# Kernel tuning notes

Measured on AMD Instinct MI355X. Metric: run time of the kernel, lower is better.

## Reference

```python
import jax, jax.numpy as jnp
import numpy as np

ALPHA = 1.5
DIM = -1
N_ITER = 50


def setup_inputs() -> dict:
    key = jax.random.key(0)
    X = jax.random.normal(key, (4096, 32000), dtype=jnp.float32)
    return {"X": X}


def reference(X):
    alpha = ALPHA
    d = X.shape[DIM]
    inv = 1.0 / (alpha - 1.0)  # exponent 1/(alpha-1)

    max_val = jnp.max(X, axis=DIM, keepdims=True)
    Xs = X * (alpha - 1.0)
    max_val = max_val * (alpha - 1.0)

    tau_lo = max_val - 1.0
    tau_hi = max_val - (1.0 / d) ** (alpha - 1.0)
    dm = tau_hi - tau_lo

    def body(i, carry):
        tau_lo, dm, _ = carry
        dm = dm * 0.5
        tau_m = tau_lo + dm
        p_m = jnp.clip(Xs - tau_m, 0.0) ** inv
        f_m = jnp.sum(p_m, axis=DIM, keepdims=True) - 1.0
        tau_lo = jnp.where(f_m >= 0.0, tau_m, tau_lo)
        return (tau_lo, dm, tau_m)

    tau_lo, dm, tau_m = jax.lax.fori_loop(0, N_ITER, body, (tau_lo, dm, tau_lo))
    # p_m from the last iteration's tau_m (matches torch loop semantics)
    p_m = jnp.clip(Xs - tau_m, 0.0) ** inv
    # ensure_sum_one=True
    p_m = p_m / jnp.sum(p_m, axis=DIM, keepdims=True)
    return p_m
```

## Files before the change

### kernel.cpp

```cpp
#include <hip/hip_runtime.h>
#include <cstdint>
#include <cstddef>


#define DLEN    32000
#define NCHUNK  8000
#define BLOCK   1024
#define PER_T   8
#define RPB     16
#define GRID_B  256
#define CAP     2048

__device__ __forceinline__ void async_copy16(void* lds_dst, const void* gsrc) {
  __builtin_amdgcn_global_load_lds(
      (const __attribute__((address_space(1))) void*)gsrc,
      (__attribute__((address_space(3))) void*)lds_dst,
      16, 0, 0);
}

__global__ __launch_bounds__(BLOCK) void entmax_bisect_kernel(
    const float* __restrict__ X, float* __restrict__ out) {
  __shared__ alignas(16) float rowbuf[DLEN];
  __shared__ float cand[CAP];
  __shared__ float wmax[BLOCK / 64];
  __shared__ int   cnt;

  const int t    = threadIdx.x;
  const int lane = t & 63;
  const int blk  = blockIdx.x;

  {
    const float* src = X + (size_t)blk * DLEN;
#pragma unroll
    for (int j = 0; j < PER_T; ++j) {
      const int c = t + j * BLOCK;
      if (c < NCHUNK) async_copy16(&rowbuf[c * 4], src + (size_t)c * 4);
    }
  }

  for (int r = 0; r < RPB; ++r) {
    const size_t row = (size_t)blk + (size_t)r * GRID_B;

    asm volatile("s_waitcnt vmcnt(0)" ::: "memory");
    __syncthreads();

    float4 v[PER_T];
#pragma unroll
    for (int j = 0; j < PER_T; ++j) {
      const int c = t + j * BLOCK;
      if (c < NCHUNK) {
        float4 q = *reinterpret_cast<const float4*>(&rowbuf[c * 4]);
        q.x *= 0.5f; q.y *= 0.5f; q.z *= 0.5f; q.w *= 0.5f;
        v[j] = q;
      } else {
        v[j] = make_float4(-3.4e38f, -3.4e38f, -3.4e38f, -3.4e38f);
      }
    }
    __syncthreads();

    if (t == 0) cnt = 0;

    if (r + 1 < RPB) {
      const float* src = X + ((size_t)blk + (size_t)(r + 1) * GRID_B) * DLEN;
#pragma unroll
      for (int j = 0; j < PER_T; ++j) {
        const int c = t + j * BLOCK;
        if (c < NCHUNK) async_copy16(&rowbuf[c * 4], src + (size_t)c * 4);
      }
    }

    float m = -3.4e38f;
#pragma unroll
    for (int j = 0; j < PER_T; ++j)
      m = fmaxf(m, fmaxf(fmaxf(v[j].x, v[j].y), fmaxf(v[j].z, v[j].w)));
#pragma unroll
    for (int off = 32; off > 0; off >>= 1) m = fmaxf(m, __shfl_xor(m, off));
    if (lane == 0) wmax[t >> 6] = m;
    __syncthreads();

    float ms = wmax[0];
#pragma unroll
    for (int w = 1; w < BLOCK / 64; ++w) ms = fmaxf(ms, wmax[w]);

    const float tlo0 = ms - 1.0f;

#pragma unroll
    for (int j = 0; j < PER_T; ++j) {
      if (v[j].x > tlo0) { int i = atomicAdd(&cnt, 1); if (i < CAP) cand[i] = v[j].x; }
      if (v[j].y > tlo0) { int i = atomicAdd(&cnt, 1); if (i < CAP) cand[i] = v[j].y; }
      if (v[j].z > tlo0) { int i = atomicAdd(&cnt, 1); if (i < CAP) cand[i] = v[j].z; }
      if (v[j].w > tlo0) { int i = atomicAdd(&cnt, 1); if (i < CAP) cand[i] = v[j].w; }
    }
    __syncthreads();

    int nc = cnt;
    if (nc > CAP) nc = CAP;

    float tau_lo = tlo0;
    float dm     = (ms - 0.0055901699437494745f) - tau_lo;
    float tau_m  = tau_lo;

#pragma unroll 1
    for (int it = 0; it < 50; ++it) {
      dm *= 0.5f;
      tau_m = tau_lo + dm;
      float s = 0.0f;
      for (int k = lane; k < nc; k += 64) {
        float d0 = fmaxf(cand[k] - tau_m, 0.0f);
        s += d0 * d0;
      }
#pragma unroll
      for (int off = 32; off > 0; off >>= 1) s += __shfl_xor(s, off);
      if (s - 1.0f >= 0.0f) tau_lo = tau_m;
      if (it < 49 && (tau_lo + dm * 0.5f == tau_lo)) { tau_m = tau_lo; break; }
    }

    float s = 0.0f;
    for (int k = lane; k < nc; k += 64) {
      float d0 = fmaxf(cand[k] - tau_m, 0.0f);
      s += d0 * d0;
    }
#pragma unroll
    for (int off = 32; off > 0; off >>= 1) s += __shfl_xor(s, off);
    const float inv_sum = 1.0f / s;

    float* dst = out + row * DLEN;
#pragma unroll
    for (int j = 0; j < PER_T; ++j) {
      const int c = t + j * BLOCK;
      if (c < NCHUNK) {
        const float4 q = v[j];
        float4 o;
        float d0;
        d0 = q.x - tau_m; o.x = (d0 > 0.0f) ? d0 * d0 * inv_sum : 0.0f;
        d0 = q.y - tau_m; o.y = (d0 > 0.0f) ? d0 * d0 * inv_sum : 0.0f;
        d0 = q.z - tau_m; o.z = (d0 > 0.0f) ? d0 * d0 * inv_sum : 0.0f;
        d0 = q.w - tau_m; o.w = (d0 > 0.0f) ? d0 * d0 * inv_sum : 0.0f;
        *reinterpret_cast<float4*>(dst + (size_t)c * 4) = o;
      }
    }
  }
}

extern "C" void kernel_launch(void* const* d_in, const int* in_sizes, int n_in,
                              void* d_out, int out_size, void* d_ws, size_t ws_size,
                              hipStream_t stream) {
  (void)in_sizes; (void)n_in; (void)d_ws; (void)ws_size; (void)out_size;
  const float* X = (const float*)d_in[0];
  float* out = (float*)d_out;
  entmax_bisect_kernel<<<dim3(GRID_B), dim3(BLOCK), 0, stream>>>(X, out);
}
```

Measured before the change: 1.080 ms.

## Replace LDS row prefetch with direct loads, doubled grid, and wave-scan candidate compaction

Drops the async global-to-LDS row prefetch and loads each row straight into registers. The grid doubles to 512 blocks with 8 rows each, and the 125KB row buffer is gone, so LDS use per block shrinks and more blocks can be resident. Candidate compaction now counts per thread, runs a wave prefix scan and issues one LDS atomic per wave, replacing one atomic per element. The change gives up explicit prefetch overlap and relies on occupancy to hide load latency. It also raises the candidate cap.

```diff
diff --git a/kernel.cpp b/kernel.cpp
--- a/kernel.cpp
+++ b/kernel.cpp
@@ -3,93 +3,79 @@
 #include <cstddef>
 
 
-#define DLEN    32000
-#define NCHUNK  8000
-#define BLOCK   1024
-#define PER_T   8
-#define RPB     16
-#define GRID_B  256
-#define CAP     2048
+#define DLEN   32000
+#define NCH    8000
+#define BLOCK  1024
+#define PER_T  8
+#define GRID_B 512
+#define RPB    8
+#define CAP    6144
 
-__device__ __forceinline__ void async_copy16(void* lds_dst, const void* gsrc) {
-  __builtin_amdgcn_global_load_lds(
-      (const __attribute__((address_space(1))) void*)gsrc,
-      (__attribute__((address_space(3))) void*)lds_dst,
-      16, 0, 0);
-}
-
-__global__ __launch_bounds__(BLOCK) void entmax_bisect_kernel(
+__global__ __launch_bounds__(BLOCK, 8) void entmax_bisect_kernel(
     const float* __restrict__ X, float* __restrict__ out) {
-  __shared__ alignas(16) float rowbuf[DLEN];
   __shared__ float cand[CAP];
-  __shared__ float wmax[BLOCK / 64];
+  __shared__ float wred[BLOCK / 64];
   __shared__ int   cnt;
 
   const int t    = threadIdx.x;
   const int lane = t & 63;
-  const int blk  = blockIdx.x;
-
-  {
-    const float* src = X + (size_t)blk * DLEN;
-#pragma unroll
-    for (int j = 0; j < PER_T; ++j) {
-      const int c = t + j * BLOCK;
-      if (c < NCHUNK) async_copy16(&rowbuf[c * 4], src + (size_t)c * 4);
-    }
-  }
+  const int wid  = t >> 6;
 
   for (int r = 0; r < RPB; ++r) {
-    const size_t row = (size_t)blk + (size_t)r * GRID_B;
-
-    asm volatile("s_waitcnt vmcnt(0)" ::: "memory");
-    __syncthreads();
+    const size_t row = (size_t)blockIdx.x + (size_t)r * GRID_B;
+    const float4* __restrict__ src =
+        reinterpret_cast<const float4*>(X + row * (size_t)DLEN);
 
     float4 v[PER_T];
 #pragma unroll
     for (int j = 0; j < PER_T; ++j) {
       const int c = t + j * BLOCK;
-      if (c < NCHUNK) {
-        float4 q = *reinterpret_cast<const float4*>(&rowbuf[c * 4]);
+      if (c < NCH) {
+        float4 q = src[c];
         q.x *= 0.5f; q.y *= 0.5f; q.z *= 0.5f; q.w *= 0.5f;
         v[j] = q;
       } else {
-        v[j] = make_float4(-3.4e38f, -3.4e38f, -3.4e38f, -3.4e38f);
-      }
-    }
-    __syncthreads();
-
-    if (t == 0) cnt = 0;
-
-    if (r + 1 < RPB) {
-      const float* src = X + ((size_t)blk + (size_t)(r + 1) * GRID_B) * DLEN;
-#pragma unroll
-      for (int j = 0; j < PER_T; ++j) {
-        const int c = t + j * BLOCK;
-        if (c < NCHUNK) async_copy16(&rowbuf[c * 4], src + (size_t)c * 4);
+        v[j] = make_float4(-3.0e38f, -3.0e38f, -3.0e38f, -3.0e38f);
       }
     }
 
-    float m = -3.4e38f;
+    float m = -3.0e38f;
 #pragma unroll
     for (int j = 0; j < PER_T; ++j)
       m = fmaxf(m, fmaxf(fmaxf(v[j].x, v[j].y), fmaxf(v[j].z, v[j].w)));
 #pragma unroll
     for (int off = 32; off > 0; off >>= 1) m = fmaxf(m, __shfl_xor(m, off));
-    if (lane == 0) wmax[t >> 6] = m;
+    if (lane == 0) wred[wid] = m;
+    if (t == 0) cnt = 0;
     __syncthreads();
 
-    float ms = wmax[0];
+    float ms = wred[0];
 #pragma unroll
-    for (int w = 1; w < BLOCK / 64; ++w) ms = fmaxf(ms, wmax[w]);
+    for (int w = 1; w < BLOCK / 64; ++w) ms = fmaxf(ms, wred[w]);
+    const float tlo0 = ms - 1.0f;
 
-    const float tlo0 = ms - 1.0f;
+    int mcnt = 0;
+#pragma unroll
+    for (int j = 0; j < PER_T; ++j)
+      mcnt += (v[j].x > tlo0) + (v[j].y > tlo0) + (v[j].z > tlo0) + (v[j].w > tlo0);
+
+    int scan = mcnt;
+#pragma unroll
+    for (int off = 1; off < 64; off <<= 1) {
+      int n = __shfl_up(scan, off);
+      if (lane >= off) scan += n;
+    }
+    int base = 0;
+    if (lane == 63 && scan > 0) base = atomicAdd(&cnt, scan);
+    base = __shfl(base, 63);
+    int pos = base + scan - mcnt;
 
 #pragma unroll
     for (int j = 0; j < PER_T; ++j) {
-      if (v[j].x > tlo0) { int i = atomicAdd(&cnt, 1); if (i < CAP) cand[i] = v[j].x; }
-      if (v[j].y > tlo0) { int i = atomicAdd(&cnt, 1); if (i < CAP) cand[i] = v[j].y; }
-      if (v[j].z > tlo0) { int i = atomicAdd(&cnt, 1); if (i < CAP) cand[i] = v[j].z; }
-      if (v[j].w > tlo0) { int i = atomicAdd(&cnt, 1); if (i < CAP) cand[i] = v[j].w; }
+      if (v[j].x > tlo0) { if (pos < CAP) cand[pos] = v[j].x; ++pos; }
+      if (v[j].y > tlo0) { if (pos < CAP) cand[pos] = v[j].y; ++pos; }
+      if (v[j].z > tlo0) { if (pos < CAP) cand[pos] = v[j].z; ++pos; }
+      if (v[j].w > tlo0) { if (pos < CAP) cand[pos] = v[j].w; ++pos; }
     }
     __syncthreads();
 
@@ -107,36 +93,35 @@
       float s = 0.0f;
       for (int k = lane; k < nc; k += 64) {
         float d0 = fmaxf(cand[k] - tau_m, 0.0f);
-        s += d0 * d0;
+        s = fmaf(d0, d0, s);
       }
 #pragma unroll
       for (int off = 32; off > 0; off >>= 1) s += __shfl_xor(s, off);
-      if (s - 1.0f >= 0.0f) tau_lo = tau_m;
+      if (s >= 1.0f) tau_lo = tau_m;
       if (it < 49 && (tau_lo + dm * 0.5f == tau_lo)) { tau_m = tau_lo; break; }
     }
 
     float s = 0.0f;
     for (int k = lane; k < nc; k += 64) {
       float d0 = fmaxf(cand[k] - tau_m, 0.0f);
-      s += d0 * d0;
+      s = fmaf(d0, d0, s);
     }
 #pragma unroll
     for (int off = 32; off > 0; off >>= 1) s += __shfl_xor(s, off);
     const float inv_sum = 1.0f / s;
 
-    float* dst = out + row * DLEN;
+    float4* __restrict__ dst = reinterpret_cast<float4*>(out + row * (size_t)DLEN);
 #pragma unroll
     for (int j = 0; j < PER_T; ++j) {
       const int c = t + j * BLOCK;
-      if (c < NCHUNK) {
+      if (c < NCH) {
         const float4 q = v[j];
-        float4 o;
-        float d0;
+        float4 o; float d0;
         d0 = q.x - tau_m; o.x = (d0 > 0.0f) ? d0 * d0 * inv_sum : 0.0f;
         d0 = q.y - tau_m; o.y = (d0 > 0.0f) ? d0 * d0 * inv_sum : 0.0f;
         d0 = q.z - tau_m; o.z = (d0 > 0.0f) ? d0 * d0 * inv_sum : 0.0f;
         d0 = q.w - tau_m; o.w = (d0 > 0.0f) ? d0 * d0 * inv_sum : 0.0f;
-        *reinterpret_cast<float4*>(dst + (size_t)c * 4) = o;
+        dst[c] = o;
       }
     }
   }
```

After: 963.1 us. 10.8% less time.
